# Optimization experiments

Measured on AMD Instinct MI355X. Metric: run time of the kernel, lower is better.

## Reference

```python
import jax, jax.numpy as jnp
import numpy as np

NUM_IDS = 8          # label ids 0..7; id 0 is background (skipped)
DD = 2.5


def setup_inputs() -> dict:
    key = jax.random.key(0)
    k1, k2 = jax.random.split(key)
    embedding_space = jax.random.normal(k1, (8, 32, 512, 512), dtype=jnp.float32)
    label = jax.random.randint(k2, (8, 1, 512, 512), 0, NUM_IDS, dtype=jnp.int32)
    return {"embedding_space": embedding_space, "label": label}


def _per_image_loss(e, l):
    # e: [HW, C] float, l: [HW] int
    sums = jax.ops.segment_sum(e, l, num_segments=NUM_IDS)                 # [K, C]
    counts = jax.ops.segment_sum(jnp.ones(e.shape[0], e.dtype), l,
                                 num_segments=NUM_IDS)                     # [K]
    means = sums / counts[:, None]                                         # [K, C]
    # per-pixel distance to its cluster mean
    d = jnp.sqrt(jnp.sum((e - means[l]) ** 2, axis=-1))                    # [HW]
    per_class_mean_dist = jax.ops.segment_sum(d, l, num_segments=NUM_IDS) / counts
    var_loss = jnp.sum(per_class_mean_dist[1:])       # skip background id 0

    m = means[1:]                                      # [K-1, C] foreground cluster means
    n_clusters = NUM_IDS - 1
    diff = m[:, None, :] - m[None, :, :]
    sq = jnp.sum(diff * diff, axis=-1)                 # [K-1, K-1]
    upper = jnp.triu(jnp.ones((n_clusters, n_clusters), bool), k=1)
    dist = jnp.sqrt(jnp.where(upper, sq, 1.0))         # safe sqrt off-pairs
    hinge = jnp.where(upper & (dist < 2.0 * DD), (2.0 * DD - dist) ** 2, 0.0)
    dist_loss = jnp.sum(hinge) / (n_clusters - 1)
    return (var_loss + dist_loss) / n_clusters


def reference(embedding_space, label):
    b, c, h, w = embedding_space.shape
    emb = embedding_space.transpose(0, 2, 3, 1).reshape(b, h * w, c)  # [B, HW, C]
    lab = label.reshape(b, h * w)                                     # [B, HW]
    losses = jax.vmap(_per_image_loss)(emb, lab)                      # [B]
    return jnp.mean(losses).reshape(1)
```

## Files before the change

kernel.cpp:

```cpp
#include <hip/hip_runtime.h>

#define HW 262144
#define NB 8
#define NC 32
#define NK 8

#define WS_PSUM 0
#define WS_PCNT 32768
#define WS_MT   33792
#define WS_CNT  35840
#define WS_PD   35904

typedef float f4 __attribute__((ext_vector_type(4)));

__global__ __launch_bounds__(256) void k_pass1(const float* __restrict__ emb,
                                               const int* __restrict__ lab,
                                               float* __restrict__ ws) {
    __shared__ float slots[256 * 9];
    __shared__ float red[256];
    const int t = threadIdx.x;
    const int f = blockIdx.x;
    const int b = f & 7;
    const int o = f >> 3;
    const int chunk = o >> 5;
    const int c = o & 31;

    float* myslot = &slots[t * 9];
#pragma unroll
    for (int i = 0; i < 9; ++i) myslot[i] = 0.f;

    const float* e = emb + ((size_t)(b * NC + c)) * HW;
    const int* lb = lab + (size_t)b * HW;
    const int base = chunk * 16384;

    for (int it = 0; it < 16; ++it) {
        const int p = base + it * 1024 + t * 4;
        const int4 l4 = *reinterpret_cast<const int4*>(lb + p);
        const f4 e4 = __builtin_nontemporal_load(reinterpret_cast<const f4*>(e + p));
        myslot[l4.x] += e4.x;
        myslot[l4.y] += e4.y;
        myslot[l4.z] += e4.z;
        myslot[l4.w] += e4.w;
    }
    __syncthreads();

    {
        const int k = t & 7, r = t >> 3;
        float s = 0.f;
#pragma unroll
        for (int i = 0; i < 8; ++i) s += slots[(r + 32 * i) * 9 + k];
        red[r * 8 + k] = s;
    }
    __syncthreads();
    if (t < 8) {
        float s = 0.f;
#pragma unroll
        for (int r = 0; r < 32; ++r) s += red[r * 8 + t];
        ws[WS_PSUM + ((size_t)f) * 8 + t] = s;
    }

    if (c == 0) {
        __syncthreads();
#pragma unroll
        for (int i = 0; i < 9; ++i) myslot[i] = 0.f;
        for (int it = 0; it < 16; ++it) {
            const int p = base + it * 1024 + t * 4;
            const int4 l4 = *reinterpret_cast<const int4*>(lb + p);
            myslot[l4.x] += 1.f;
            myslot[l4.y] += 1.f;
            myslot[l4.z] += 1.f;
            myslot[l4.w] += 1.f;
        }
        __syncthreads();
        {
            const int k = t & 7, r = t >> 3;
            float s = 0.f;
#pragma unroll
            for (int i = 0; i < 8; ++i) s += slots[(r + 32 * i) * 9 + k];
            red[r * 8 + k] = s;
        }
        __syncthreads();
        if (t < 8) {
            float s = 0.f;
#pragma unroll
            for (int r = 0; r < 32; ++r) s += red[r * 8 + t];
            ws[WS_PCNT + (b * 16 + chunk) * 8 + t] = s;
        }
    }
}

__global__ __launch_bounds__(256) void k_means(float* __restrict__ ws) {
    const int b = blockIdx.x;
    const int t = threadIdx.x;
    const int c = t >> 3, k = t & 7;

    float cnt = 0.f;
#pragma unroll
    for (int ch = 0; ch < 16; ++ch) cnt += ws[WS_PCNT + (b * 16 + ch) * 8 + k];

    float s = 0.f;
#pragma unroll
    for (int ch = 0; ch < 16; ++ch) s += ws[WS_PSUM + ((size_t)(b + 8 * (c + 32 * ch))) * 8 + k];

    ws[WS_MT + b * 256 + c * 8 + k] = s / cnt;
    if (c == 0) ws[WS_CNT + b * 8 + k] = cnt;
}

__global__ __launch_bounds__(256) void k_dist(const float* __restrict__ emb,
                                              const int* __restrict__ lab,
                                              float* __restrict__ ws) {
    __shared__ float mT[256];
    __shared__ float slots[256 * 9];
    __shared__ float red[256];
    const int t = threadIdx.x;
    const int f = blockIdx.x;
    const int b = f & 7;
    const int chunk = f >> 3;

    mT[t] = ws[WS_MT + b * 256 + t];
    float* myslot = &slots[t * 9];
#pragma unroll
    for (int i = 0; i < 9; ++i) myslot[i] = 0.f;
    __syncthreads();

    const int p = chunk * 1024 + t * 4;
    const int4 l4 = *reinterpret_cast<const int4*>(lab + (size_t)b * HW + p);
    const float* e = emb + (size_t)b * NC * HW + p;

    float a0 = 0.f, a1 = 0.f, a2 = 0.f, a3 = 0.f;
#pragma unroll 8
    for (int c = 0; c < NC; ++c) {
        const f4 e4 = __builtin_nontemporal_load(reinterpret_cast<const f4*>(e + (size_t)c * HW));
        const float* mrow = &mT[c * 8];
        float d0 = e4.x - mrow[l4.x];
        float d1 = e4.y - mrow[l4.y];
        float d2 = e4.z - mrow[l4.z];
        float d3 = e4.w - mrow[l4.w];
        a0 += d0 * d0;
        a1 += d1 * d1;
        a2 += d2 * d2;
        a3 += d3 * d3;
    }
    myslot[l4.x] += sqrtf(a0);
    myslot[l4.y] += sqrtf(a1);
    myslot[l4.z] += sqrtf(a2);
    myslot[l4.w] += sqrtf(a3);
    __syncthreads();

    {
        const int k = t & 7, r = t >> 3;
        float s = 0.f;
#pragma unroll
        for (int i = 0; i < 8; ++i) s += slots[(r + 32 * i) * 9 + k];
        red[r * 8 + k] = s;
    }
    __syncthreads();
    if (t < 8) {
        float s = 0.f;
#pragma unroll
        for (int r = 0; r < 32; ++r) s += red[r * 8 + t];
        ws[WS_PD + ((size_t)f) * 8 + t] = s;
    }
}

__global__ __launch_bounds__(256) void k_final(const float* __restrict__ ws,
                                               float* __restrict__ out) {
    __shared__ float partial[256];
    __shared__ float distsum[64];
    __shared__ float varl[8];
    __shared__ float hingeL[8 * 21];
    __shared__ float distl[8];
    const int t = threadIdx.x;

    {
        const int pidx = t >> 2;
        const int sub = t & 3;
        float s = 0.f;
        for (int j = 0; j < 64; ++j)
            s += ws[WS_PD + (size_t)(j * 4 + sub) * 64 + pidx];
        partial[t] = s;
    }
    __syncthreads();
    if (t < 64)
        distsum[t] = partial[t * 4] + partial[t * 4 + 1] + partial[t * 4 + 2] + partial[t * 4 + 3];
    __syncthreads();

    if (t < 8) {
        float v = 0.f;
#pragma unroll
        for (int k = 1; k < 8; ++k)
            v += distsum[t * 8 + k] / ws[WS_CNT + t * 8 + k];
        varl[t] = v;
    }

    if (t < 168) {
        const int b = t / 21;
        const int pr = t - b * 21;
        int ii = 1, jj = 2, cnt = 0;
        for (int a = 1; a <= 7; ++a)
            for (int bb = a + 1; bb <= 7; ++bb) {
                if (cnt == pr) { ii = a; jj = bb; }
                ++cnt;
            }
        const float* mTb = ws + WS_MT + b * 256;
        float sq = 0.f;
#pragma unroll
        for (int c = 0; c < NC; ++c) {
            const float d = mTb[c * 8 + ii] - mTb[c * 8 + jj];
            sq += d * d;
        }
        const float dist = sqrtf(sq);
        const float gap = 5.0f - dist;
        hingeL[t] = (dist < 5.0f) ? gap * gap : 0.f;
    }
    __syncthreads();
    if (t < 8) {
        float h = 0.f;
#pragma unroll
        for (int pr = 0; pr < 21; ++pr) h += hingeL[t * 21 + pr];
        distl[t] = h;
    }
    __syncthreads();
    if (t == 0) {
        float s = 0.f;
#pragma unroll
        for (int b = 0; b < 8; ++b)
            s += (varl[b] + distl[b] * (1.0f / 6.0f)) * (1.0f / 7.0f);
        out[0] = s * 0.125f;
    }
}

extern "C" void kernel_launch(void* const* d_in, const int* in_sizes, int n_in,
                              void* d_out, int out_size, void* d_ws, size_t ws_size,
                              hipStream_t stream) {
    const float* emb = (const float*)d_in[0];
    const int* lab = (const int*)d_in[1];
    float* out = (float*)d_out;
    float* ws = (float*)d_ws;

    k_pass1<<<NB * 16 * NC, 256, 0, stream>>>(emb, lab, ws);
    k_means<<<NB, 256, 0, stream>>>(ws);
    k_dist<<<NB * 256, 256, 0, stream>>>(emb, lab, ws);
    k_final<<<1, 256, 0, stream>>>(ws, out);
}
```

Measured before the change: 103.5 us.

## Cache FP8 embedding copy and packed labels in pass1 for second pass

The first pass now writes an FP8 (e4m3) copy of the embeddings and byte-packed labels into workspace, and the distance pass reads these smaller buffers instead of re-reading fp32 embeddings and int32 labels. The aim is to cut memory traffic in the second pass by roughly a factor of four. In exchange, pass one gains extra stores, and distances are computed from FP8-quantised values, which adds error to the variance term. It falls back to the fp32 path when the workspace is too small.

```diff
diff --git a/kernel.cpp b/kernel.cpp
--- a/kernel.cpp
+++ b/kernel.cpp
@@ -5,17 +5,25 @@
 #define NC 32
 #define NK 8
 
-#define WS_PSUM 0
-#define WS_PCNT 32768
-#define WS_MT   33792
-#define WS_CNT  35840
-#define WS_PD   35904
-
 typedef float f4 __attribute__((ext_vector_type(4)));
-
+typedef float v2f __attribute__((ext_vector_type(2)));
+
+#define OFF_F8   ((size_t)0)
+#define OFF_PL   ((size_t)67108864)
+#define OFF_PSUM ((size_t)69206016)
+#define OFF_PCNT ((size_t)69337088)
+#define OFF_MT   ((size_t)69341184)
+#define OFF_CNT  ((size_t)69349376)
+#define OFF_PD   ((size_t)69349632)
+#define WS_NEED  ((size_t)69415168)
+
+template <bool FP8>
 __global__ __launch_bounds__(256) void k_pass1(const float* __restrict__ emb,
                                                const int* __restrict__ lab,
-                                               float* __restrict__ ws) {
+                                               float* __restrict__ psum,
+                                               float* __restrict__ pcnt,
+                                               unsigned char* __restrict__ f8,
+                                               unsigned char* __restrict__ plab) {
     __shared__ float slots[256 * 9];
     __shared__ float red[256];
     const int t = threadIdx.x;
@@ -31,12 +39,18 @@
 
     const float* e = emb + ((size_t)(b * NC + c)) * HW;
     const int* lb = lab + (size_t)b * HW;
+    unsigned char* f8c = FP8 ? (f8 + ((size_t)(b * NC + c)) * HW) : nullptr;
     const int base = chunk * 16384;
 
     for (int it = 0; it < 16; ++it) {
         const int p = base + it * 1024 + t * 4;
         const int4 l4 = *reinterpret_cast<const int4*>(lb + p);
         const f4 e4 = __builtin_nontemporal_load(reinterpret_cast<const f4*>(e + p));
+        if (FP8) {
+            int w = __builtin_amdgcn_cvt_pk_fp8_f32(e4.x, e4.y, 0, false);
+            w = __builtin_amdgcn_cvt_pk_fp8_f32(e4.z, e4.w, w, true);
+            *reinterpret_cast<int*>(f8c + p) = w;
+        }
         myslot[l4.x] += e4.x;
         myslot[l4.y] += e4.y;
         myslot[l4.z] += e4.z;
@@ -56,7 +70,7 @@
         float s = 0.f;
 #pragma unroll
         for (int r = 0; r < 32; ++r) s += red[r * 8 + t];
-        ws[WS_PSUM + ((size_t)f) * 8 + t] = s;
+        psum[(size_t)f * 8 + t] = s;
     }
 
     if (c == 0) {
@@ -66,6 +80,11 @@
         for (int it = 0; it < 16; ++it) {
             const int p = base + it * 1024 + t * 4;
             const int4 l4 = *reinterpret_cast<const int4*>(lb + p);
+            if (FP8) {
+                const unsigned int pl = (unsigned)l4.x | ((unsigned)l4.y << 8) |
+                                        ((unsigned)l4.z << 16) | ((unsigned)l4.w << 24);
+                *reinterpret_cast<unsigned int*>(plab + (size_t)b * HW + p) = pl;
+            }
             myslot[l4.x] += 1.f;
             myslot[l4.y] += 1.f;
             myslot[l4.z] += 1.f;
@@ -84,31 +103,35 @@
             float s = 0.f;
 #pragma unroll
             for (int r = 0; r < 32; ++r) s += red[r * 8 + t];
-            ws[WS_PCNT + (b * 16 + chunk) * 8 + t] = s;
-        }
-    }
-}
-
-__global__ __launch_bounds__(256) void k_means(float* __restrict__ ws) {
+            pcnt[(b * 16 + chunk) * 8 + t] = s;
+        }
+    }
+}
+
+__global__ __launch_bounds__(256) void k_means(const float* __restrict__ psum,
+                                               const float* __restrict__ pcnt,
+                                               float* __restrict__ mt,
+                                               float* __restrict__ cnt) {
     const int b = blockIdx.x;
     const int t = threadIdx.x;
     const int c = t >> 3, k = t & 7;
 
-    float cnt = 0.f;
-#pragma unroll
-    for (int ch = 0; ch < 16; ++ch) cnt += ws[WS_PCNT + (b * 16 + ch) * 8 + k];
+    float cn = 0.f;
+#pragma unroll
+    for (int ch = 0; ch < 16; ++ch) cn += pcnt[(b * 16 + ch) * 8 + k];
 
     float s = 0.f;
 #pragma unroll
-    for (int ch = 0; ch < 16; ++ch) s += ws[WS_PSUM + ((size_t)(b + 8 * (c + 32 * ch))) * 8 + k];
-
-    ws[WS_MT + b * 256 + c * 8 + k] = s / cnt;
-    if (c == 0) ws[WS_CNT + b * 8 + k] = cnt;
-}
-
-__global__ __launch_bounds__(256) void k_dist(const float* __restrict__ emb,
-                                              const int* __restrict__ lab,
-                                              float* __restrict__ ws) {
+    for (int ch = 0; ch < 16; ++ch) s += psum[(size_t)(b + 8 * (c + 32 * ch)) * 8 + k];
+
+    mt[b * 256 + c * 8 + k] = s / cn;
+    if (c == 0) cnt[b * 8 + k] = cn;
+}
+
+__global__ __launch_bounds__(256) void k_dist_fp8(const unsigned char* __restrict__ f8,
+                                                  const unsigned char* __restrict__ plab,
+                                                  const float* __restrict__ mt,
+                                                  float* __restrict__ pd) {
     __shared__ float mT[256];
     __shared__ float slots[256 * 9];
     __shared__ float red[256];
@@ -117,7 +140,68 @@
     const int b = f & 7;
     const int chunk = f >> 3;
 
-    mT[t] = ws[WS_MT + b * 256 + t];
+    mT[t] = mt[b * 256 + t];
+    float* myslot = &slots[t * 9];
+#pragma unroll
+    for (int i = 0; i < 9; ++i) myslot[i] = 0.f;
+    __syncthreads();
+
+    const int p = chunk * 1024 + t * 4;
+    const unsigned int lw = *reinterpret_cast<const unsigned int*>(plab + (size_t)b * HW + p);
+    const int l0 = lw & 0xff, l1 = (lw >> 8) & 0xff, l2 = (lw >> 16) & 0xff, l3 = lw >> 24;
+    const unsigned char* e8 = f8 + (size_t)b * NC * HW + p;
+
+    float a0 = 0.f, a1 = 0.f, a2 = 0.f, a3 = 0.f;
+#pragma unroll 8
+    for (int c = 0; c < NC; ++c) {
+        const unsigned int ew = *reinterpret_cast<const unsigned int*>(e8 + (size_t)c * HW);
+        const v2f lo = __builtin_amdgcn_cvt_pk_f32_fp8(ew, false);
+        const v2f hi = __builtin_amdgcn_cvt_pk_f32_fp8(ew, true);
+        const float* mrow = &mT[c * 8];
+        const float d0 = lo.x - mrow[l0];
+        const float d1 = lo.y - mrow[l1];
+        const float d2 = hi.x - mrow[l2];
+        const float d3 = hi.y - mrow[l3];
+        a0 += d0 * d0;
+        a1 += d1 * d1;
+        a2 += d2 * d2;
+        a3 += d3 * d3;
+    }
+    myslot[l0] += sqrtf(a0);
+    myslot[l1] += sqrtf(a1);
+    myslot[l2] += sqrtf(a2);
+    myslot[l3] += sqrtf(a3);
+    __syncthreads();
+
+    {
+        const int k = t & 7, r = t >> 3;
+        float s = 0.f;
+#pragma unroll
+        for (int i = 0; i < 8; ++i) s += slots[(r + 32 * i) * 9 + k];
+        red[r * 8 + k] = s;
+    }
+    __syncthreads();
+    if (t < 8) {
+        float s = 0.f;
+#pragma unroll
+        for (int r = 0; r < 32; ++r) s += red[r * 8 + t];
+        pd[(size_t)f * 8 + t] = s;
+    }
+}
+
+__global__ __launch_bounds__(256) void k_dist_f32(const float* __restrict__ emb,
+                                                  const int* __restrict__ lab,
+                                                  const float* __restrict__ mt,
+                                                  float* __restrict__ pd) {
+    __shared__ float mT[256];
+    __shared__ float slots[256 * 9];
+    __shared__ float red[256];
+    const int t = threadIdx.x;
+    const int f = blockIdx.x;
+    const int b = f & 7;
+    const int chunk = f >> 3;
+
+    mT[t] = mt[b * 256 + t];
     float* myslot = &slots[t * 9];
 #pragma unroll
     for (int i = 0; i < 9; ++i) myslot[i] = 0.f;
@@ -132,10 +216,10 @@
     for (int c = 0; c < NC; ++c) {
         const f4 e4 = __builtin_nontemporal_load(reinterpret_cast<const f4*>(e + (size_t)c * HW));
         const float* mrow = &mT[c * 8];
-        float d0 = e4.x - mrow[l4.x];
-        float d1 = e4.y - mrow[l4.y];
-        float d2 = e4.z - mrow[l4.z];
-        float d3 = e4.w - mrow[l4.w];
+        const float d0 = e4.x - mrow[l4.x];
+        const float d1 = e4.y - mrow[l4.y];
+        const float d2 = e4.z - mrow[l4.z];
+        const float d3 = e4.w - mrow[l4.w];
         a0 += d0 * d0;
         a1 += d1 * d1;
         a2 += d2 * d2;
@@ -159,50 +243,48 @@
         float s = 0.f;
 #pragma unroll
         for (int r = 0; r < 32; ++r) s += red[r * 8 + t];
-        ws[WS_PD + ((size_t)f) * 8 + t] = s;
-    }
-}
-
-__global__ __launch_bounds__(256) void k_final(const float* __restrict__ ws,
+        pd[(size_t)f * 8 + t] = s;
+    }
+}
+
+__global__ __launch_bounds__(256) void k_final(const float* __restrict__ pd,
+                                               const float* __restrict__ cnt,
+                                               const float* __restrict__ mt,
                                                float* __restrict__ out) {
     __shared__ float partial[256];
     __shared__ float distsum[64];
     __shared__ float varl[8];
     __shared__ float hingeL[8 * 21];
-    __shared__ float distl[8];
     const int t = threadIdx.x;
 
     {
-        const int pidx = t >> 2;
-        const int sub = t & 3;
-        float s = 0.f;
-        for (int j = 0; j < 64; ++j)
-            s += ws[WS_PD + (size_t)(j * 4 + sub) * 64 + pidx];
+        float s = 0.f;
+        for (int j = 0; j < 64; ++j) s += pd[(size_t)j * 256 + t];
         partial[t] = s;
     }
     __syncthreads();
     if (t < 64)
-        distsum[t] = partial[t * 4] + partial[t * 4 + 1] + partial[t * 4 + 2] + partial[t * 4 + 3];
+        distsum[t] = partial[t] + partial[t + 64] + partial[t + 128] + partial[t + 192];
     __syncthreads();
 
     if (t < 8) {
         float v = 0.f;
 #pragma unroll
         for (int k = 1; k < 8; ++k)
-            v += distsum[t * 8 + k] / ws[WS_CNT + t * 8 + k];
+            v += distsum[t * 8 + k] / cnt[t * 8 + k];
         varl[t] = v;
     }
 
     if (t < 168) {
         const int b = t / 21;
         const int pr = t - b * 21;
-        int ii = 1, jj = 2, cnt = 0;
+        int ii = 1, jj = 2, c2 = 0;
         for (int a = 1; a <= 7; ++a)
             for (int bb = a + 1; bb <= 7; ++bb) {
-                if (cnt == pr) { ii = a; jj = bb; }
-                ++cnt;
+                if (c2 == pr) { ii = a; jj = bb; }
+                ++c2;
             }
-        const float* mTb = ws + WS_MT + b * 256;
+        const float* mTb = mt + b * 256;
         float sq = 0.f;
 #pragma unroll
         for (int c = 0; c < NC; ++c) {
@@ -214,18 +296,14 @@
         hingeL[t] = (dist < 5.0f) ? gap * gap : 0.f;
     }
     __syncthreads();
-    if (t < 8) {
-        float h = 0.f;
-#pragma unroll
-        for (int pr = 0; pr < 21; ++pr) h += hingeL[t * 21 + pr];
-        distl[t] = h;
-    }
-    __syncthreads();
     if (t == 0) {
         float s = 0.f;
 #pragma unroll
-        for (int b = 0; b < 8; ++b)
-            s += (varl[b] + distl[b] * (1.0f / 6.0f)) * (1.0f / 7.0f);
+        for (int b = 0; b < 8; ++b) {
+            float h = 0.f;
+            for (int pr = 0; pr < 21; ++pr) h += hingeL[b * 21 + pr];
+            s += (varl[b] + h * (1.0f / 6.0f)) * (1.0f / 7.0f);
+        }
         out[0] = s * 0.125f;
     }
 }
@@ -236,10 +314,31 @@
     const float* emb = (const float*)d_in[0];
     const int* lab = (const int*)d_in[1];
     float* out = (float*)d_out;
-    float* ws = (float*)d_ws;
-
-    k_pass1<<<NB * 16 * NC, 256, 0, stream>>>(emb, lab, ws);
-    k_means<<<NB, 256, 0, stream>>>(ws);
-    k_dist<<<NB * 256, 256, 0, stream>>>(emb, lab, ws);
-    k_final<<<1, 256, 0, stream>>>(ws, out);
-}
+    unsigned char* ws8 = (unsigned char*)d_ws;
+
+    if (ws_size >= WS_NEED) {
+        unsigned char* f8 = ws8 + OFF_F8;
+        unsigned char* pl = ws8 + OFF_PL;
+        float* psum = (float*)(ws8 + OFF_PSUM);
+        float* pcnt = (float*)(ws8 + OFF_PCNT);
+        float* mt = (float*)(ws8 + OFF_MT);
+        float* cnt = (float*)(ws8 + OFF_CNT);
+        float* pd = (float*)(ws8 + OFF_PD);
+
+        k_pass1<true><<<NB * 16 * NC, 256, 0, stream>>>(emb, lab, psum, pcnt, f8, pl);
+        k_means<<<NB, 256, 0, stream>>>(psum, pcnt, mt, cnt);
+        k_dist_fp8<<<NB * 256, 256, 0, stream>>>(f8, pl, mt, pd);
+        k_final<<<1, 256, 0, stream>>>(pd, cnt, mt, out);
+    } else {
+        float* psum = (float*)ws8;
+        float* pcnt = psum + 32768;
+        float* mt = pcnt + 1024;
+        float* cnt = mt + 2048;
+        float* pd = cnt + 64;
+
+        k_pass1<false><<<NB * 16 * NC, 256, 0, stream>>>(emb, lab, psum, pcnt, nullptr, nullptr);
+        k_means<<<NB, 256, 0, stream>>>(psum, pcnt, mt, cnt);
+        k_dist_f32<<<NB * 256, 256, 0, stream>>>(emb, lab, mt, pd);
+        k_final<<<1, 256, 0, stream>>>(pd, cnt, mt, out);
+    }
+}
```

New measurement: 95.33 us. -7.9%, faster.

## Cache fp8 copy of embeddings in pass1 for cheaper distance pass; fuse final

Applied to the files above, without the earlier changes.

Pass 1 now writes an FP8-compressed copy of each embedding channel into workspace (as many channels as the workspace allows). The distance pass then reads those bytes instead of the fp32 data, cutting its second read of the full tensor to about a quarter. The final reduction is folded into the distance kernel through an atomic last-block counter, and label counting is spread across eight channel blocks. The distance kernel also handles eight pixels per thread with a transposed means layout. The fp8 path costs extra writes in pass 1 and introduces quantisation error into the per-pixel distances, so the loss is no longer computed exactly.

```diff
diff --git a/kernel.cpp b/kernel.cpp
--- a/kernel.cpp
+++ b/kernel.cpp
@@ -4,18 +4,26 @@
 #define NB 8
 #define NC 32
 #define NK 8
-
-#define WS_PSUM 0
-#define WS_PCNT 32768
-#define WS_MT   33792
-#define WS_CNT  35840
-#define WS_PD   35904
+#define DIST_BLOCKS 1024
 
 typedef float f4 __attribute__((ext_vector_type(4)));
+typedef float v2f __attribute__((ext_vector_type(2)));
+typedef unsigned int uv2 __attribute__((ext_vector_type(2)));
+
+#define OFF_PSUM ((size_t)0)
+#define OFF_PCNT ((size_t)131072)
+#define OFF_MT   ((size_t)163840)
+#define OFF_CNT  ((size_t)173056)
+#define OFF_PD   ((size_t)173312)
+#define OFF_CTR  ((size_t)206080)
+#define OFF_F8   ((size_t)(1 << 20))
 
 __global__ __launch_bounds__(256) void k_pass1(const float* __restrict__ emb,
                                                const int* __restrict__ lab,
-                                               float* __restrict__ ws) {
+                                               float* __restrict__ psum,
+                                               float* __restrict__ pcnt,
+                                               unsigned char* __restrict__ f8,
+                                               int ncomp) {
     __shared__ float slots[256 * 9];
     __shared__ float red[256];
     const int t = threadIdx.x;
@@ -32,11 +40,17 @@
     const float* e = emb + ((size_t)(b * NC + c)) * HW;
     const int* lb = lab + (size_t)b * HW;
     const int base = chunk * 16384;
+    unsigned char* f8c = (c < ncomp) ? (f8 + ((size_t)(b * ncomp + c)) * HW) : nullptr;
 
     for (int it = 0; it < 16; ++it) {
         const int p = base + it * 1024 + t * 4;
         const int4 l4 = *reinterpret_cast<const int4*>(lb + p);
         const f4 e4 = __builtin_nontemporal_load(reinterpret_cast<const f4*>(e + p));
+        if (f8c) {
+            int w = __builtin_amdgcn_cvt_pk_fp8_f32(e4.x, e4.y, 0, false);
+            w = __builtin_amdgcn_cvt_pk_fp8_f32(e4.z, e4.w, w, true);
+            *reinterpret_cast<int*>(f8c + p) = w;
+        }
         myslot[l4.x] += e4.x;
         myslot[l4.y] += e4.y;
         myslot[l4.z] += e4.z;
@@ -56,21 +70,20 @@
         float s = 0.f;
 #pragma unroll
         for (int r = 0; r < 32; ++r) s += red[r * 8 + t];
-        ws[WS_PSUM + ((size_t)f) * 8 + t] = s;
-    }
-
-    if (c == 0) {
+        psum[(size_t)f * 8 + t] = s;
+    }
+
+    if (c < 8) {
         __syncthreads();
 #pragma unroll
         for (int i = 0; i < 9; ++i) myslot[i] = 0.f;
-        for (int it = 0; it < 16; ++it) {
-            const int p = base + it * 1024 + t * 4;
-            const int4 l4 = *reinterpret_cast<const int4*>(lb + p);
-            myslot[l4.x] += 1.f;
-            myslot[l4.y] += 1.f;
-            myslot[l4.z] += 1.f;
-            myslot[l4.w] += 1.f;
-        }
+        const int sb = base + c * 2048 + t * 8;
+        const int4 la = *reinterpret_cast<const int4*>(lb + sb);
+        const int4 lc = *reinterpret_cast<const int4*>(lb + sb + 4);
+        myslot[la.x] += 1.f; myslot[la.y] += 1.f;
+        myslot[la.z] += 1.f; myslot[la.w] += 1.f;
+        myslot[lc.x] += 1.f; myslot[lc.y] += 1.f;
+        myslot[lc.z] += 1.f; myslot[lc.w] += 1.f;
         __syncthreads();
         {
             const int k = t & 7, r = t >> 3;
@@ -84,67 +97,151 @@
             float s = 0.f;
 #pragma unroll
             for (int r = 0; r < 32; ++r) s += red[r * 8 + t];
-            ws[WS_PCNT + (b * 16 + chunk) * 8 + t] = s;
+            pcnt[((size_t)((b * 16 + chunk) * 8 + c)) * 8 + t] = s;
         }
     }
 }
 
-__global__ __launch_bounds__(256) void k_means(float* __restrict__ ws) {
+__global__ __launch_bounds__(256) void k_means(const float* __restrict__ psum,
+                                               const float* __restrict__ pcnt,
+                                               float* __restrict__ mt2,
+                                               float* __restrict__ cnt,
+                                               unsigned int* __restrict__ ctr) {
+    __shared__ float red[256];
+    __shared__ float csh[8];
     const int b = blockIdx.x;
     const int t = threadIdx.x;
-    const int c = t >> 3, k = t & 7;
-
-    float cnt = 0.f;
-#pragma unroll
-    for (int ch = 0; ch < 16; ++ch) cnt += ws[WS_PCNT + (b * 16 + ch) * 8 + k];
-
-    float s = 0.f;
-#pragma unroll
-    for (int ch = 0; ch < 16; ++ch) s += ws[WS_PSUM + ((size_t)(b + 8 * (c + 32 * ch))) * 8 + k];
-
-    ws[WS_MT + b * 256 + c * 8 + k] = s / cnt;
-    if (c == 0) ws[WS_CNT + b * 8 + k] = cnt;
+    const int hi3 = t >> 3, k = t & 7;
+
+    {
+        float s = 0.f;
+#pragma unroll
+        for (int j = 0; j < 4; ++j)
+            s += pcnt[(size_t)(b * 128 + hi3 * 4 + j) * 8 + k];
+        red[t] = s;
+    }
+    __syncthreads();
+    if (t < 8) {
+        float cn = 0.f;
+#pragma unroll
+        for (int i = 0; i < 32; ++i) cn += red[i * 8 + t];
+        csh[t] = cn;
+        cnt[b * 8 + t] = cn;
+    }
+    __syncthreads();
+
+    float ssum = 0.f;
+#pragma unroll
+    for (int ch = 0; ch < 16; ++ch)
+        ssum += psum[(size_t)(b + 8 * (hi3 + 32 * ch)) * 8 + k];
+    mt2[b * 288 + k * 36 + hi3] = ssum / csh[k];
+
+    if (b == 0 && t == 0) *ctr = 0u;
 }
 
 __global__ __launch_bounds__(256) void k_dist(const float* __restrict__ emb,
                                               const int* __restrict__ lab,
-                                              float* __restrict__ ws) {
-    __shared__ float mT[256];
+                                              const unsigned char* __restrict__ f8,
+                                              const float* __restrict__ mt2,
+                                              const float* __restrict__ cnt,
+                                              float* __restrict__ pd,
+                                              unsigned int* __restrict__ ctr,
+                                              float* __restrict__ out,
+                                              int ncomp) {
+    __shared__ float mTs[288];
     __shared__ float slots[256 * 9];
     __shared__ float red[256];
+    __shared__ float ds2[64];
+    __shared__ float vv[8];
+    __shared__ float hi2[168];
+    __shared__ unsigned int lastFlag;
     const int t = threadIdx.x;
     const int f = blockIdx.x;
     const int b = f & 7;
-    const int chunk = f >> 3;
-
-    mT[t] = ws[WS_MT + b * 256 + t];
+    const int cb = f >> 3;
+
+    mTs[t] = mt2[b * 288 + t];
+    if (t < 32) mTs[256 + t] = mt2[b * 288 + 256 + t];
     float* myslot = &slots[t * 9];
 #pragma unroll
     for (int i = 0; i < 9; ++i) myslot[i] = 0.f;
     __syncthreads();
 
-    const int p = chunk * 1024 + t * 4;
-    const int4 l4 = *reinterpret_cast<const int4*>(lab + (size_t)b * HW + p);
-    const float* e = emb + (size_t)b * NC * HW + p;
+    const int p0 = cb * 2048 + t * 8;
+    const int4 la = *reinterpret_cast<const int4*>(lab + (size_t)b * HW + p0);
+    const int4 lb4 = *reinterpret_cast<const int4*>(lab + (size_t)b * HW + p0 + 4);
+    const int l0 = la.x, l1 = la.y, l2 = la.z, l3 = la.w;
+    const int l4_ = lb4.x, l5 = lb4.y, l6 = lb4.z, l7 = lb4.w;
 
     float a0 = 0.f, a1 = 0.f, a2 = 0.f, a3 = 0.f;
-#pragma unroll 8
-    for (int c = 0; c < NC; ++c) {
-        const f4 e4 = __builtin_nontemporal_load(reinterpret_cast<const f4*>(e + (size_t)c * HW));
-        const float* mrow = &mT[c * 8];
-        float d0 = e4.x - mrow[l4.x];
-        float d1 = e4.y - mrow[l4.y];
-        float d2 = e4.z - mrow[l4.z];
-        float d3 = e4.w - mrow[l4.w];
-        a0 += d0 * d0;
-        a1 += d1 * d1;
-        a2 += d2 * d2;
-        a3 += d3 * d3;
-    }
-    myslot[l4.x] += sqrtf(a0);
-    myslot[l4.y] += sqrtf(a1);
-    myslot[l4.z] += sqrtf(a2);
-    myslot[l4.w] += sqrtf(a3);
+    float a4 = 0.f, a5 = 0.f, a6 = 0.f, a7 = 0.f;
+
+    const unsigned char* e8 = f8 + (size_t)(b * ncomp) * HW + p0;
+    for (int cg = 0; cg < ncomp; cg += 4) {
+        const f4 m0 = *reinterpret_cast<const f4*>(&mTs[l0 * 36 + cg]);
+        const f4 m1 = *reinterpret_cast<const f4*>(&mTs[l1 * 36 + cg]);
+        const f4 m2 = *reinterpret_cast<const f4*>(&mTs[l2 * 36 + cg]);
+        const f4 m3 = *reinterpret_cast<const f4*>(&mTs[l3 * 36 + cg]);
+        const f4 m4 = *reinterpret_cast<const f4*>(&mTs[l4_ * 36 + cg]);
+        const f4 m5 = *reinterpret_cast<const f4*>(&mTs[l5 * 36 + cg]);
+        const f4 m6 = *reinterpret_cast<const f4*>(&mTs[l6 * 36 + cg]);
+        const f4 m7 = *reinterpret_cast<const f4*>(&mTs[l7 * 36 + cg]);
+#pragma unroll
+        for (int cc = 0; cc < 4; ++cc) {
+            const uv2 ew = __builtin_nontemporal_load(
+                reinterpret_cast<const uv2*>(e8 + (size_t)(cg + cc) * HW));
+            const v2f p01 = __builtin_amdgcn_cvt_pk_f32_fp8(ew.x, false);
+            const v2f p23 = __builtin_amdgcn_cvt_pk_f32_fp8(ew.x, true);
+            const v2f p45 = __builtin_amdgcn_cvt_pk_f32_fp8(ew.y, false);
+            const v2f p67 = __builtin_amdgcn_cvt_pk_f32_fp8(ew.y, true);
+            float d;
+            d = p01.x - m0[cc]; a0 += d * d;
+            d = p01.y - m1[cc]; a1 += d * d;
+            d = p23.x - m2[cc]; a2 += d * d;
+            d = p23.y - m3[cc]; a3 += d * d;
+            d = p45.x - m4[cc]; a4 += d * d;
+            d = p45.y - m5[cc]; a5 += d * d;
+            d = p67.x - m6[cc]; a6 += d * d;
+            d = p67.y - m7[cc]; a7 += d * d;
+        }
+    }
+
+    const float* ef = emb + (size_t)(b * NC) * HW + p0;
+    for (int cg = ncomp; cg < 32; cg += 4) {
+        const f4 m0 = *reinterpret_cast<const f4*>(&mTs[l0 * 36 + cg]);
+        const f4 m1 = *reinterpret_cast<const f4*>(&mTs[l1 * 36 + cg]);
+        const f4 m2 = *reinterpret_cast<const f4*>(&mTs[l2 * 36 + cg]);
+        const f4 m3 = *reinterpret_cast<const f4*>(&mTs[l3 * 36 + cg]);
+        const f4 m4 = *reinterpret_cast<const f4*>(&mTs[l4_ * 36 + cg]);
+        const f4 m5 = *reinterpret_cast<const f4*>(&mTs[l5 * 36 + cg]);
+        const f4 m6 = *reinterpret_cast<const f4*>(&mTs[l6 * 36 + cg]);
+        const f4 m7 = *reinterpret_cast<const f4*>(&mTs[l7 * 36 + cg]);
+#pragma unroll
+        for (int cc = 0; cc < 4; ++cc) {
+            const f4 ea = __builtin_nontemporal_load(
+                reinterpret_cast<const f4*>(ef + (size_t)(cg + cc) * HW));
+            const f4 eb = __builtin_nontemporal_load(
+                reinterpret_cast<const f4*>(ef + (size_t)(cg + cc) * HW + 4));
+            float d;
+            d = ea.x - m0[cc]; a0 += d * d;
+            d = ea.y - m1[cc]; a1 += d * d;
+            d = ea.z - m2[cc]; a2 += d * d;
+            d = ea.w - m3[cc]; a3 += d * d;
+            d = eb.x - m4[cc]; a4 += d * d;
+            d = eb.y - m5[cc]; a5 += d * d;
+            d = eb.z - m6[cc]; a6 += d * d;
+            d = eb.w - m7[cc]; a7 += d * d;
+        }
+    }
+
+    myslot[l0] += sqrtf(a0);
+    myslot[l1] += sqrtf(a1);
+    myslot[l2] += sqrtf(a2);
+    myslot[l3] += sqrtf(a3);
+    myslot[l4_] += sqrtf(a4);
+    myslot[l5] += sqrtf(a5);
+    myslot[l6] += sqrtf(a6);
+    myslot[l7] += sqrtf(a7);
     __syncthreads();
 
     {
@@ -159,73 +256,67 @@
         float s = 0.f;
 #pragma unroll
         for (int r = 0; r < 32; ++r) s += red[r * 8 + t];
-        ws[WS_PD + ((size_t)f) * 8 + t] = s;
-    }
-}
-
-__global__ __launch_bounds__(256) void k_final(const float* __restrict__ ws,
-                                               float* __restrict__ out) {
-    __shared__ float partial[256];
-    __shared__ float distsum[64];
-    __shared__ float varl[8];
-    __shared__ float hingeL[8 * 21];
-    __shared__ float distl[8];
-    const int t = threadIdx.x;
+        pd[(size_t)f * 8 + t] = s;
+    }
+    __syncthreads();
+
+    if (t == 0) {
+        __threadfence();
+        lastFlag = (atomicAdd(ctr, 1u) == DIST_BLOCKS - 1) ? 1u : 0u;
+    }
+    __syncthreads();
+    if (lastFlag == 0u) return;
+    if (t == 0) __threadfence();
+    __syncthreads();
 
     {
-        const int pidx = t >> 2;
-        const int sub = t & 3;
-        float s = 0.f;
-        for (int j = 0; j < 64; ++j)
-            s += ws[WS_PD + (size_t)(j * 4 + sub) * 64 + pidx];
-        partial[t] = s;
+        const int pr = t >> 2, sub = t & 3;
+        const int bq = pr >> 3, kq = pr & 7;
+        float s = 0.f;
+        for (int j = sub; j < 128; j += 4)
+            s += pd[(size_t)(bq + 8 * j) * 8 + kq];
+        red[t] = s;
     }
     __syncthreads();
     if (t < 64)
-        distsum[t] = partial[t * 4] + partial[t * 4 + 1] + partial[t * 4 + 2] + partial[t * 4 + 3];
-    __syncthreads();
-
+        ds2[t] = red[t * 4] + red[t * 4 + 1] + red[t * 4 + 2] + red[t * 4 + 3];
+    __syncthreads();
     if (t < 8) {
         float v = 0.f;
 #pragma unroll
         for (int k = 1; k < 8; ++k)
-            v += distsum[t * 8 + k] / ws[WS_CNT + t * 8 + k];
-        varl[t] = v;
-    }
-
+            v += ds2[t * 8 + k] / cnt[t * 8 + k];
+        vv[t] = v;
+    }
     if (t < 168) {
-        const int b = t / 21;
-        const int pr = t - b * 21;
-        int ii = 1, jj = 2, cnt = 0;
+        const int bb = t / 21;
+        const int pr = t - bb * 21;
+        int ii = 1, jj = 2, c2 = 0;
         for (int a = 1; a <= 7; ++a)
-            for (int bb = a + 1; bb <= 7; ++bb) {
-                if (cnt == pr) { ii = a; jj = bb; }
-                ++cnt;
+            for (int b2 = a + 1; b2 <= 7; ++b2) {
+                if (c2 == pr) { ii = a; jj = b2; }
+                ++c2;
             }
-        const float* mTb = ws + WS_MT + b * 256;
+        const float* mTb = mt2 + bb * 288;
         float sq = 0.f;
 #pragma unroll
         for (int c = 0; c < NC; ++c) {
-            const float d = mTb[c * 8 + ii] - mTb[c * 8 + jj];
+            const float d = mTb[ii * 36 + c] - mTb[jj * 36 + c];
             sq += d * d;
         }
         const float dist = sqrtf(sq);
         const float gap = 5.0f - dist;
-        hingeL[t] = (dist < 5.0f) ? gap * gap : 0.f;
-    }
-    __syncthreads();
-    if (t < 8) {
-        float h = 0.f;
-#pragma unroll
-        for (int pr = 0; pr < 21; ++pr) h += hingeL[t * 21 + pr];
-        distl[t] = h;
+        hi2[t] = (dist < 5.0f) ? gap * gap : 0.f;
     }
     __syncthreads();
     if (t == 0) {
         float s = 0.f;
 #pragma unroll
-        for (int b = 0; b < 8; ++b)
-            s += (varl[b] + distl[b] * (1.0f / 6.0f)) * (1.0f / 7.0f);
+        for (int bb = 0; bb < 8; ++bb) {
+            float h = 0.f;
+            for (int pr = 0; pr < 21; ++pr) h += hi2[bb * 21 + pr];
+            s += (vv[bb] + h * (1.0f / 6.0f)) * (1.0f / 7.0f);
+        }
         out[0] = s * 0.125f;
     }
 }
@@ -236,10 +327,24 @@
     const float* emb = (const float*)d_in[0];
     const int* lab = (const int*)d_in[1];
     float* out = (float*)d_out;
-    float* ws = (float*)d_ws;
-
-    k_pass1<<<NB * 16 * NC, 256, 0, stream>>>(emb, lab, ws);
-    k_means<<<NB, 256, 0, stream>>>(ws);
-    k_dist<<<NB * 256, 256, 0, stream>>>(emb, lab, ws);
-    k_final<<<1, 256, 0, stream>>>(ws, out);
+    unsigned char* w = (unsigned char*)d_ws;
+
+    int ncomp = 0;
+    if (ws_size > OFF_F8) {
+        size_t avail = (ws_size - OFF_F8) / ((size_t)NB * HW);
+        ncomp = (int)(avail > 32 ? 32 : avail);
+        ncomp &= ~3;
+    }
+
+    float* psum = (float*)(w + OFF_PSUM);
+    float* pcnt = (float*)(w + OFF_PCNT);
+    float* mt2  = (float*)(w + OFF_MT);
+    float* cnt  = (float*)(w + OFF_CNT);
+    float* pd   = (float*)(w + OFF_PD);
+    unsigned int* ctr = (unsigned int*)(w + OFF_CTR);
+    unsigned char* f8 = w + OFF_F8;
+
+    k_pass1<<<4096, 256, 0, stream>>>(emb, lab, psum, pcnt, f8, ncomp);
+    k_means<<<NB, 256, 0, stream>>>(psum, pcnt, mt2, cnt, ctr);
+    k_dist<<<DIST_BLOCKS, 256, 0, stream>>>(emb, lab, f8, mt2, cnt, pd, ctr, out, ncomp);
 }
```

New measurement: 119.0 us. 14.9% more time.
